# Kernel optimization log

Measured on AMD Instinct MI355X. Metric: run time of the kernel, lower is better.

Reference implementation:

```python
import jax, jax.numpy as jnp
import numpy as np

DELTA = 1e-3  # kernel_delta

B, N, D, K = 256, 131072, 128, 50


def setup_inputs() -> dict:
    key = jax.random.key(0)
    k1, k2, k3 = jax.random.split(key, 3)
    return {
        "key": jax.random.normal(k1, (B, D), dtype=jnp.float32),
        "keys": jax.random.normal(k2, (N, D), dtype=jnp.float32),
        "values": jax.random.normal(k3, (N, 1), dtype=jnp.float32),
        "num_neighbours": K,
    }


def reference(key, keys, values, num_neighbours):
    # Squared L2 distance via GEMM expansion (same math as
    # torch.square(torch.norm(key[:,None]-keys, dim=-1)))
    q_sq = jnp.sum(key * key, axis=1, keepdims=True)          # [B,1]
    d_sq = jnp.sum(keys * keys, axis=1)                        # [N]
    cross = key @ keys.T                                       # [B,N] GEMM
    dist2 = jnp.maximum(q_sq + d_sq[None, :] - 2.0 * cross, 0.0)
    # inverse-distance-weighting kernel
    weights = 1.0 / (dist2 + DELTA)                            # [B,N]
    # top-k mask + renormalize (non-topk weights are zeroed, so the
    # normalized sum reduces to a sum over the top-k entries)
    top_w, top_idx = jax.lax.top_k(weights, num_neighbours)    # [B,K]
    w_norm = top_w / jnp.sum(top_w, axis=1, keepdims=True)     # [B,K]
    # gather matched values and weighted sum
    v = values[top_idx, 0]                                     # [B,K]
    output = jnp.sum(w_norm * v, axis=1, keepdims=True)        # [B,1]
    return output
```

## Files before the change

kernel.cpp:

```cpp
#include <hip/hip_runtime.h>

#define BQ 256
#define NK 131072
#define DIM 128
#define KT2 128
#define NCH2 (NK / KT2)
#define DELTA 1e-3f

#define NB 8192
#define SHIFT 18
#define CAP 2048

typedef __attribute__((ext_vector_type(8))) short bf16x8;
typedef __attribute__((ext_vector_type(4))) float f32x4;

__device__ __forceinline__ unsigned short f2bf(float x) {
    unsigned u = __float_as_uint(x);
    u += 0x7fffu + ((u >> 16) & 1u);
    return (unsigned short)(u >> 16);
}
__device__ __forceinline__ float bf2f(unsigned short h) {
    return __uint_as_float(((unsigned)h) << 16);
}

__global__ __launch_bounds__(256, 4)
void p0_qsq(const float* __restrict__ qkey, float* __restrict__ qsqg)
{
    const int t = threadIdx.x;
    #pragma unroll 1
    for (int p = 0; p < 16; ++p) {
        int r  = p * 16 + (t >> 4);
        int d0 = (t & 15) * 8;
        const float* src = qkey + (r << 7) + d0;
        float4 a = *(const float4*)src, b = *(const float4*)(src + 4);
        float s = (a.x*a.x + a.y*a.y) + (a.z*a.z + a.w*a.w)
                + (b.x*b.x + b.y*b.y) + (b.z*b.z + b.w*b.w);
        #pragma unroll
        for (int off = 1; off < 16; off <<= 1) s += __shfl_xor(s, off, 16);
        if ((t & 15) == 0) qsqg[r] = s;
    }
}

__global__ __launch_bounds__(512, 2)
void p1_mfma(const float* __restrict__ qkey, const float* __restrict__ keys,
             const float* __restrict__ qsqg, float* __restrict__ dist,
             int q0, int nq)
{
    __shared__ __align__(16) unsigned short khs[KT2 * DIM];
    __shared__ __align__(16) unsigned short kls[KT2 * DIM];
    __shared__ float ksq_s[KT2];
    __shared__ float qsq_s[BQ];

    const int tid   = threadIdx.x;
    const int kbase = blockIdx.x * KT2;

    if (tid < BQ) qsq_s[tid] = qsqg[tid];

    #pragma unroll
    for (int p = 0; p < 4; ++p) {
        int flat = p * 4096 + tid * 8;
        int rr = flat >> 7;
        int d0 = flat & 127;
        const float* src = keys + (((size_t)(kbase + rr)) << 7) + d0;
        float4 a = *(const float4*)src, b = *(const float4*)(src + 4);
        float xs0 = a.x, xs1 = a.y, xs2 = a.z, xs3 = a.w;
        float xs4 = b.x, xs5 = b.y, xs6 = b.z, xs7 = b.w;
        bf16x8 hv, lv;
        unsigned short h;
        h = f2bf(xs0); hv[0] = (short)h; lv[0] = (short)f2bf(xs0 - bf2f(h));
        h = f2bf(xs1); hv[1] = (short)h; lv[1] = (short)f2bf(xs1 - bf2f(h));
        h = f2bf(xs2); hv[2] = (short)h; lv[2] = (short)f2bf(xs2 - bf2f(h));
        h = f2bf(xs3); hv[3] = (short)h; lv[3] = (short)f2bf(xs3 - bf2f(h));
        h = f2bf(xs4); hv[4] = (short)h; lv[4] = (short)f2bf(xs4 - bf2f(h));
        h = f2bf(xs5); hv[5] = (short)h; lv[5] = (short)f2bf(xs5 - bf2f(h));
        h = f2bf(xs6); hv[6] = (short)h; lv[6] = (short)f2bf(xs6 - bf2f(h));
        h = f2bf(xs7); hv[7] = (short)h; lv[7] = (short)f2bf(xs7 - bf2f(h));
        float sq = (xs0*xs0 + xs1*xs1) + (xs2*xs2 + xs3*xs3)
                 + (xs4*xs4 + xs5*xs5) + (xs6*xs6 + xs7*xs7);
        unsigned byte = (unsigned)((rr << 8) + (d0 << 1));
        byte ^= (unsigned)((rr & 7) << 4);
        *(bf16x8*)((char*)khs + byte) = hv;
        *(bf16x8*)((char*)kls + byte) = lv;
        #pragma unroll
        for (int off = 1; off < 16; off <<= 1) sq += __shfl_xor(sq, off, 16);
        if ((tid & 15) == 0) ksq_s[rr] = sq;
    }

    const int lane = tid & 63, wv = tid >> 6;
    const int qb0 = wv * 32;
    const int fr = lane & 15, fg = lane >> 4;
    bf16x8 qh[2][4], ql[2][4];
    #pragma unroll
    for (int qf = 0; qf < 2; ++qf)
        #pragma unroll
        for (int s = 0; s < 4; ++s) {
            const float* qp = qkey + ((size_t)(qb0 + qf * 16 + fr) << 7) + s * 32 + fg * 8;
            float4 a = *(const float4*)qp, b = *(const float4*)(qp + 4);
            float x0 = a.x, x1 = a.y, x2 = a.z, x3 = a.w;
            float x4 = b.x, x5 = b.y, x6 = b.z, x7 = b.w;
            bf16x8 hv, lv;
            unsigned short h;
            h = f2bf(x0); hv[0] = (short)h; lv[0] = (short)f2bf(x0 - bf2f(h));
            h = f2bf(x1); hv[1] = (short)h; lv[1] = (short)f2bf(x1 - bf2f(h));
            h = f2bf(x2); hv[2] = (short)h; lv[2] = (short)f2bf(x2 - bf2f(h));
            h = f2bf(x3); hv[3] = (short)h; lv[3] = (short)f2bf(x3 - bf2f(h));
            h = f2bf(x4); hv[4] = (short)h; lv[4] = (short)f2bf(x4 - bf2f(h));
            h = f2bf(x5); hv[5] = (short)h; lv[5] = (short)f2bf(x5 - bf2f(h));
            h = f2bf(x6); hv[6] = (short)h; lv[6] = (short)f2bf(x6 - bf2f(h));
            h = f2bf(x7); hv[7] = (short)h; lv[7] = (short)f2bf(x7 - bf2f(h));
            qh[qf][s] = hv; ql[qf][s] = lv;
        }

    f32x4 acc[2][8];
    #pragma unroll
    for (int qf = 0; qf < 2; ++qf)
        #pragma unroll
        for (int kf = 0; kf < 8; ++kf) acc[qf][kf] = f32x4{0.f, 0.f, 0.f, 0.f};

    __syncthreads();

    #pragma unroll
    for (int s = 0; s < 4; ++s) {
        #pragma unroll
        for (int kf = 0; kf < 8; ++kf) {
            const int krow = kf * 16 + fr;
            const int d0   = s * 32 + fg * 8;
            unsigned byte = ((unsigned)((krow << 8) + (d0 << 1))) ^ (unsigned)((krow & 7) << 4);
            bf16x8 bh = *(bf16x8*)((char*)khs + byte);
            bf16x8 bl = *(bf16x8*)((char*)kls + byte);
            #pragma unroll
            for (int qf = 0; qf < 2; ++qf) {
                acc[qf][kf] = __builtin_amdgcn_mfma_f32_16x16x32_bf16(qh[qf][s], bh, acc[qf][kf], 0, 0, 0);
                acc[qf][kf] = __builtin_amdgcn_mfma_f32_16x16x32_bf16(ql[qf][s], bh, acc[qf][kf], 0, 0, 0);
                acc[qf][kf] = __builtin_amdgcn_mfma_f32_16x16x32_bf16(qh[qf][s], bl, acc[qf][kf], 0, 0, 0);
            }
        }
    }

    #pragma unroll
    for (int qf = 0; qf < 2; ++qf) {
        #pragma unroll
        for (int kf = 0; kf < 8; ++kf) {
            int k = kbase + kf * 16 + fr;
            float kq = ksq_s[kf * 16 + fr];
            f32x4 a = acc[qf][kf];
            #pragma unroll
            for (int rg = 0; rg < 4; ++rg) {
                int q = qb0 + qf * 16 + fg * 4 + rg;
                int qrel = q - q0;
                if (qrel >= 0 && qrel < nq) {
                    float dv = fmaxf(qsq_s[q] + kq - 2.f * a[rg], 0.f);
                    dist[(size_t)qrel * NK + k] = dv;
                }
            }
        }
    }
}

__global__ __launch_bounds__(1024, 1)
void p2_select(const float* __restrict__ dist,
               const float* __restrict__ values,
               const int* __restrict__ pK,
               float* __restrict__ out)
{
    const int tid  = threadIdx.x;
    const int lane = tid & 63;
    const int wid  = tid >> 6;
    const float4* row4 = (const float4*)(dist + (size_t)blockIdx.x * NK);

    int K = *pK; if (K < 1) K = 1; if (K > NK) K = NK;

    __shared__ int   hist[NB];
    __shared__ uint2 list[CAP];
    __shared__ int   lcount, s_bb, s_cb;
    __shared__ int   iscan[16];
    __shared__ float fred[48];

    for (int i = tid; i < NB; i += 1024) hist[i] = 0;
    if (tid == 0) { lcount = 0; s_bb = NB - 1; s_cb = 0; }
    __syncthreads();

    for (int i = 0; i < NK / 4096; ++i) {
        float4 v = row4[tid + 1024 * i];
        atomicAdd(&hist[__float_as_uint(v.x) >> SHIFT], 1);
        atomicAdd(&hist[__float_as_uint(v.y) >> SHIFT], 1);
        atomicAdd(&hist[__float_as_uint(v.z) >> SHIFT], 1);
        atomicAdd(&hist[__float_as_uint(v.w) >> SHIFT], 1);
    }
    __syncthreads();

    int h[8], s = 0;
    #pragma unroll
    for (int b = 0; b < 8; ++b) { h[b] = hist[tid * 8 + b]; s += h[b]; }
    int incl = s;
    #pragma unroll
    for (int off = 1; off < 64; off <<= 1) {
        int t = __shfl_up(incl, off, 64);
        if (lane >= off) incl += t;
    }
    if (lane == 63) iscan[wid] = incl;
    __syncthreads();
    if (tid == 0) { int c = 0; for (int w = 0; w < 16; ++w) { int t = iscan[w]; iscan[w] = c; c += t; } }
    __syncthreads();
    int base = iscan[wid] + (incl - s);
    if (base < K && K <= base + s) {
        int c = base;
        #pragma unroll
        for (int b = 0; b < 8; ++b) {
            if (c < K && c + h[b] >= K) { s_bb = tid * 8 + b; s_cb = c; }
            c += h[b];
        }
    }
    __syncthreads();
    const int bb = s_bb, cbelow = s_cb, R = K - cbelow, CEall = hist[bb];

    float sw = 0.f, swv = 0.f, seva = 0.f;
    for (int i = 0; i < NK / 4096; ++i) {
        float4 v = row4[tid + 1024 * i];
        int n0 = (tid + 1024 * i) * 4;
        float dd[4] = { v.x, v.y, v.z, v.w };
        #pragma unroll
        for (int c = 0; c < 4; ++c) {
            unsigned bts = __float_as_uint(dd[c]);
            int bin = (int)(bts >> SHIFT);
            if (bin < bb) {
                float w = 1.f / (dd[c] + DELTA);
                float vv = values[n0 + c];
                sw += w; swv = fmaf(w, vv, swv);
            } else if (bin == bb) {
                float vv = values[n0 + c];
                seva += vv;
                int sl = atomicAdd(&lcount, 1);
                if (sl < CAP) list[sl] = make_uint2(bts, __float_as_uint(vv));
            }
        }
    }
    #pragma unroll
    for (int off = 32; off; off >>= 1) {
        sw   += __shfl_down(sw,   off, 64);
        swv  += __shfl_down(swv,  off, 64);
        seva += __shfl_down(seva, off, 64);
    }
    if (lane == 0) { fred[wid] = sw; fred[16 + wid] = swv; fred[32 + wid] = seva; }
    __syncthreads();

    if (wid == 0) {
        float SW = 0.f, SWV = 0.f, SEVA = 0.f;
        for (int w = 0; w < 16; ++w) { SW += fred[w]; SWV += fred[16 + w]; SEVA += fred[32 + w]; }
        const int L = lcount;
        double num, den;
        if (L <= CAP) {
            unsigned lo = ((unsigned)bb) << SHIFT;
            unsigned hi = lo + ((1u << SHIFT) - 1u);
            while (lo < hi) {
                unsigned mid = lo + ((hi - lo) >> 1);
                int c = 0;
                for (int i = lane; i < L; i += 64) c += (list[i].x <= mid) ? 1 : 0;
                #pragma unroll
                for (int off = 32; off; off >>= 1) c += __shfl_xor(c, off, 64);
                if (c >= R) hi = mid; else lo = mid + 1;
            }
            const unsigned T = lo;
            int cl2 = 0, ce = 0;
            double swl = 0.0, swvl = 0.0, sevt = 0.0;
            for (int i = lane; i < L; i += 64) {
                unsigned b = list[i].x;
                float vv = __uint_as_float(list[i].y);
                if (b < T) {
                    double w = 1.0 / ((double)__uint_as_float(b) + (double)DELTA);
                    cl2 += 1; swl += w; swvl += w * (double)vv;
                } else if (b == T) { ce += 1; sevt += (double)vv; }
            }
            #pragma unroll
            for (int off = 32; off; off >>= 1) {
                cl2  += __shfl_xor(cl2,  off, 64);
                ce   += __shfl_xor(ce,   off, 64);
                swl  += __shfl_xor(swl,  off, 64);
                swvl += __shfl_xor(swvl, off, 64);
                sevt += __shfl_xor(sevt, off, 64);
            }
            const int need = R - cl2;
            double wT = 1.0 / ((double)__uint_as_float(T) + (double)DELTA);
            num = (double)SWV + swvl + wT * ((double)need / (double)ce) * sevt;
            den = (double)SW  + swl  + wT * (double)need;
        } else {
            double wT = 1.0 / ((double)__uint_as_float(((unsigned)bb) << SHIFT) + (double)DELTA);
            num = (double)SWV + wT * ((double)R / (double)CEall) * (double)SEVA;
            den = (double)SW  + wT * (double)R;
        }
        if (lane == 0) out[blockIdx.x] = (float)(num / den);
    }
}

extern "C" void kernel_launch(void* const* d_in, const int* in_sizes, int n_in,
                              void* d_out, int out_size, void* d_ws, size_t ws_size,
                              hipStream_t stream)
{
    const float* qkey   = (const float*)d_in[0];
    const float* keys   = (const float*)d_in[1];
    const float* values = (const float*)d_in[2];
    const int*   pK     = (const int*)d_in[3];
    float* out  = (float*)d_out;

    float* qsqg = (float*)d_ws;
    float* dist = (float*)d_ws + 1024;

    p0_qsq<<<dim3(1), dim3(256), 0, stream>>>(qkey, qsqg);

    const size_t rowb = (size_t)NK * sizeof(float);
    const size_t avail = ws_size - 4096;
    int slabQ = (avail >= (size_t)BQ * rowb) ? BQ : (int)(avail / rowb);
    if (slabQ < 1) slabQ = 1;

    for (int q0 = 0; q0 < BQ; q0 += slabQ) {
        int nq = BQ - q0; if (nq > slabQ) nq = slabQ;
        p1_mfma<<<dim3(NCH2), dim3(512), 0, stream>>>(qkey, keys, qsqg, dist, q0, nq);
        p2_select<<<dim3(nq), dim3(1024), 0, stream>>>(dist, values, pK, out + q0);
    }
}
```

Before: 126.2 us.

## Replace full distance matrix with sampled threshold and filtered candidate lists

```diff
diff --git a/kernel.cpp b/kernel.cpp
--- a/kernel.cpp
+++ b/kernel.cpp
@@ -5,11 +5,10 @@
 #define DIM 128
 #define KT2 128
 #define NCH2 (NK / KT2)
+#define SAMP 8192
+#define SBLK (SAMP / KT2)
+#define CAPC 16384
 #define DELTA 1e-3f
-
-#define NB 8192
-#define SHIFT 18
-#define CAP 2048
 
 typedef __attribute__((ext_vector_type(8))) short bf16x8;
 typedef __attribute__((ext_vector_type(4))) float f32x4;
@@ -22,39 +21,62 @@
 __device__ __forceinline__ float bf2f(unsigned short h) {
     return __uint_as_float(((unsigned)h) << 16);
 }
+__device__ __forceinline__ int kclamp(int K) {
+    if (K < 1) K = 1;
+    if (K > 2048) K = 2048;
+    return K;
+}
 
 __global__ __launch_bounds__(256, 4)
-void p0_qsq(const float* __restrict__ qkey, float* __restrict__ qsqg)
-{
-    const int t = threadIdx.x;
-    #pragma unroll 1
-    for (int p = 0; p < 16; ++p) {
-        int r  = p * 16 + (t >> 4);
-        int d0 = (t & 15) * 8;
-        const float* src = qkey + (r << 7) + d0;
-        float4 a = *(const float4*)src, b = *(const float4*)(src + 4);
-        float s = (a.x*a.x + a.y*a.y) + (a.z*a.z + a.w*a.w)
-                + (b.x*b.x + b.y*b.y) + (b.z*b.z + b.w*b.w);
-        #pragma unroll
-        for (int off = 1; off < 16; off <<= 1) s += __shfl_xor(s, off, 16);
-        if ((t & 15) == 0) qsqg[r] = s;
-    }
-}
-
+void p0_prep(const float* __restrict__ qkey,
+             unsigned short* __restrict__ qhG, unsigned short* __restrict__ qlG,
+             float* __restrict__ qsqg)
+{
+    const int item = blockIdx.x * 256 + threadIdx.x;
+    const int r = item >> 4, d0 = (item & 15) * 8;
+    const float* src = qkey + (r << 7) + d0;
+    float4 a = *(const float4*)src, b = *(const float4*)(src + 4);
+    float x0 = a.x, x1 = a.y, x2 = a.z, x3 = a.w;
+    float x4 = b.x, x5 = b.y, x6 = b.z, x7 = b.w;
+    bf16x8 hv, lv;
+    unsigned short h;
+    h = f2bf(x0); hv[0] = (short)h; lv[0] = (short)f2bf(x0 - bf2f(h));
+    h = f2bf(x1); hv[1] = (short)h; lv[1] = (short)f2bf(x1 - bf2f(h));
+    h = f2bf(x2); hv[2] = (short)h; lv[2] = (short)f2bf(x2 - bf2f(h));
+    h = f2bf(x3); hv[3] = (short)h; lv[3] = (short)f2bf(x3 - bf2f(h));
+    h = f2bf(x4); hv[4] = (short)h; lv[4] = (short)f2bf(x4 - bf2f(h));
+    h = f2bf(x5); hv[5] = (short)h; lv[5] = (short)f2bf(x5 - bf2f(h));
+    h = f2bf(x6); hv[6] = (short)h; lv[6] = (short)f2bf(x6 - bf2f(h));
+    h = f2bf(x7); hv[7] = (short)h; lv[7] = (short)f2bf(x7 - bf2f(h));
+    *(bf16x8*)(qhG + (r << 7) + d0) = hv;
+    *(bf16x8*)(qlG + (r << 7) + d0) = lv;
+    float s = (x0*x0 + x1*x1) + (x2*x2 + x3*x3) + (x4*x4 + x5*x5) + (x6*x6 + x7*x7);
+    #pragma unroll
+    for (int off = 1; off < 16; off <<= 1) s += __shfl_xor(s, off, 16);
+    if ((threadIdx.x & 15) == 0) qsqg[r] = s;
+}
+
+template<bool FILTER>
 __global__ __launch_bounds__(512, 2)
-void p1_mfma(const float* __restrict__ qkey, const float* __restrict__ keys,
-             const float* __restrict__ qsqg, float* __restrict__ dist,
-             int q0, int nq)
+void kmfma(const unsigned short* __restrict__ qhG, const unsigned short* __restrict__ qlG,
+           const float* __restrict__ keys, const float* __restrict__ qsqg,
+           const float* __restrict__ values, float* __restrict__ dout,
+           const unsigned* __restrict__ tau, unsigned* __restrict__ cnt,
+           uint2* __restrict__ cand)
 {
     __shared__ __align__(16) unsigned short khs[KT2 * DIM];
     __shared__ __align__(16) unsigned short kls[KT2 * DIM];
-    __shared__ float ksq_s[KT2];
-    __shared__ float qsq_s[BQ];
+    __shared__ float    ksq_s[KT2];
+    __shared__ float    qsq_s[BQ];
+    __shared__ unsigned tau_s[BQ];
 
     const int tid   = threadIdx.x;
     const int kbase = blockIdx.x * KT2;
 
-    if (tid < BQ) qsq_s[tid] = qsqg[tid];
+    if (tid < BQ) {
+        qsq_s[tid] = qsqg[tid];
+        if (FILTER) tau_s[tid] = tau[tid];
+    }
 
     #pragma unroll
     for (int p = 0; p < 4; ++p) {
@@ -63,20 +85,19 @@
         int d0 = flat & 127;
         const float* src = keys + (((size_t)(kbase + rr)) << 7) + d0;
         float4 a = *(const float4*)src, b = *(const float4*)(src + 4);
-        float xs0 = a.x, xs1 = a.y, xs2 = a.z, xs3 = a.w;
-        float xs4 = b.x, xs5 = b.y, xs6 = b.z, xs7 = b.w;
+        float x0 = a.x, x1 = a.y, x2 = a.z, x3 = a.w;
+        float x4 = b.x, x5 = b.y, x6 = b.z, x7 = b.w;
         bf16x8 hv, lv;
         unsigned short h;
-        h = f2bf(xs0); hv[0] = (short)h; lv[0] = (short)f2bf(xs0 - bf2f(h));
-        h = f2bf(xs1); hv[1] = (short)h; lv[1] = (short)f2bf(xs1 - bf2f(h));
-        h = f2bf(xs2); hv[2] = (short)h; lv[2] = (short)f2bf(xs2 - bf2f(h));
-        h = f2bf(xs3); hv[3] = (short)h; lv[3] = (short)f2bf(xs3 - bf2f(h));
-        h = f2bf(xs4); hv[4] = (short)h; lv[4] = (short)f2bf(xs4 - bf2f(h));
-        h = f2bf(xs5); hv[5] = (short)h; lv[5] = (short)f2bf(xs5 - bf2f(h));
-        h = f2bf(xs6); hv[6] = (short)h; lv[6] = (short)f2bf(xs6 - bf2f(h));
-        h = f2bf(xs7); hv[7] = (short)h; lv[7] = (short)f2bf(xs7 - bf2f(h));
-        float sq = (xs0*xs0 + xs1*xs1) + (xs2*xs2 + xs3*xs3)
-                 + (xs4*xs4 + xs5*xs5) + (xs6*xs6 + xs7*xs7);
+        h = f2bf(x0); hv[0] = (short)h; lv[0] = (short)f2bf(x0 - bf2f(h));
+        h = f2bf(x1); hv[1] = (short)h; lv[1] = (short)f2bf(x1 - bf2f(h));
+        h = f2bf(x2); hv[2] = (short)h; lv[2] = (short)f2bf(x2 - bf2f(h));
+        h = f2bf(x3); hv[3] = (short)h; lv[3] = (short)f2bf(x3 - bf2f(h));
+        h = f2bf(x4); hv[4] = (short)h; lv[4] = (short)f2bf(x4 - bf2f(h));
+        h = f2bf(x5); hv[5] = (short)h; lv[5] = (short)f2bf(x5 - bf2f(h));
+        h = f2bf(x6); hv[6] = (short)h; lv[6] = (short)f2bf(x6 - bf2f(h));
+        h = f2bf(x7); hv[7] = (short)h; lv[7] = (short)f2bf(x7 - bf2f(h));
+        float sq = (x0*x0 + x1*x1) + (x2*x2 + x3*x3) + (x4*x4 + x5*x5) + (x6*x6 + x7*x7);
         unsigned byte = (unsigned)((rr << 8) + (d0 << 1));
         byte ^= (unsigned)((rr & 7) << 4);
         *(bf16x8*)((char*)khs + byte) = hv;
@@ -94,21 +115,9 @@
     for (int qf = 0; qf < 2; ++qf)
         #pragma unroll
         for (int s = 0; s < 4; ++s) {
-            const float* qp = qkey + ((size_t)(qb0 + qf * 16 + fr) << 7) + s * 32 + fg * 8;
-            float4 a = *(const float4*)qp, b = *(const float4*)(qp + 4);
-            float x0 = a.x, x1 = a.y, x2 = a.z, x3 = a.w;
-            float x4 = b.x, x5 = b.y, x6 = b.z, x7 = b.w;
-            bf16x8 hv, lv;
-            unsigned short h;
-            h = f2bf(x0); hv[0] = (short)h; lv[0] = (short)f2bf(x0 - bf2f(h));
-            h = f2bf(x1); hv[1] = (short)h; lv[1] = (short)f2bf(x1 - bf2f(h));
-            h = f2bf(x2); hv[2] = (short)h; lv[2] = (short)f2bf(x2 - bf2f(h));
-            h = f2bf(x3); hv[3] = (short)h; lv[3] = (short)f2bf(x3 - bf2f(h));
-            h = f2bf(x4); hv[4] = (short)h; lv[4] = (short)f2bf(x4 - bf2f(h));
-            h = f2bf(x5); hv[5] = (short)h; lv[5] = (short)f2bf(x5 - bf2f(h));
-            h = f2bf(x6); hv[6] = (short)h; lv[6] = (short)f2bf(x6 - bf2f(h));
-            h = f2bf(x7); hv[7] = (short)h; lv[7] = (short)f2bf(x7 - bf2f(h));
-            qh[qf][s] = hv; ql[qf][s] = lv;
+            int off = ((qb0 + qf * 16 + fr) << 7) + s * 32 + fg * 8;
+            qh[qf][s] = *(const bf16x8*)(qhG + off);
+            ql[qf][s] = *(const bf16x8*)(qlG + off);
         }
 
     f32x4 acc[2][8];
@@ -141,154 +150,129 @@
     for (int qf = 0; qf < 2; ++qf) {
         #pragma unroll
         for (int kf = 0; kf < 8; ++kf) {
-            int k = kbase + kf * 16 + fr;
-            float kq = ksq_s[kf * 16 + fr];
+            const int kcol = kf * 16 + fr;
+            const int k = kbase + kcol;
+            const float kq = ksq_s[kcol];
             f32x4 a = acc[qf][kf];
             #pragma unroll
             for (int rg = 0; rg < 4; ++rg) {
-                int q = qb0 + qf * 16 + fg * 4 + rg;
-                int qrel = q - q0;
-                if (qrel >= 0 && qrel < nq) {
-                    float dv = fmaxf(qsq_s[q] + kq - 2.f * a[rg], 0.f);
-                    dist[(size_t)qrel * NK + k] = dv;
+                const int q = qb0 + qf * 16 + fg * 4 + rg;
+                float dv = fmaxf(qsq_s[q] + kq - 2.f * a[rg], 0.f);
+                if (FILTER) {
+                    if (dv <= __uint_as_float(tau_s[q])) {
+                        unsigned slot = atomicAdd(&cnt[q], 1u);
+                        if (slot < CAPC)
+                            cand[(size_t)q * CAPC + slot] =
+                                make_uint2(__float_as_uint(dv), __float_as_uint(values[k]));
+                    }
+                } else {
+                    dout[(size_t)q * SAMP + k] = dv;
                 }
             }
         }
     }
 }
 
-__global__ __launch_bounds__(1024, 1)
-void p2_select(const float* __restrict__ dist,
-               const float* __restrict__ values,
-               const int* __restrict__ pK,
-               float* __restrict__ out)
-{
-    const int tid  = threadIdx.x;
-    const int lane = tid & 63;
-    const int wid  = tid >> 6;
-    const float4* row4 = (const float4*)(dist + (size_t)blockIdx.x * NK);
-
-    int K = *pK; if (K < 1) K = 1; if (K > NK) K = NK;
-
-    __shared__ int   hist[NB];
-    __shared__ uint2 list[CAP];
-    __shared__ int   lcount, s_bb, s_cb;
-    __shared__ int   iscan[16];
-    __shared__ float fred[48];
-
-    for (int i = tid; i < NB; i += 1024) hist[i] = 0;
-    if (tid == 0) { lcount = 0; s_bb = NB - 1; s_cb = 0; }
-    __syncthreads();
-
-    for (int i = 0; i < NK / 4096; ++i) {
-        float4 v = row4[tid + 1024 * i];
-        atomicAdd(&hist[__float_as_uint(v.x) >> SHIFT], 1);
-        atomicAdd(&hist[__float_as_uint(v.y) >> SHIFT], 1);
-        atomicAdd(&hist[__float_as_uint(v.z) >> SHIFT], 1);
-        atomicAdd(&hist[__float_as_uint(v.w) >> SHIFT], 1);
-    }
-    __syncthreads();
-
-    int h[8], s = 0;
-    #pragma unroll
-    for (int b = 0; b < 8; ++b) { h[b] = hist[tid * 8 + b]; s += h[b]; }
-    int incl = s;
-    #pragma unroll
-    for (int off = 1; off < 64; off <<= 1) {
-        int t = __shfl_up(incl, off, 64);
-        if (lane >= off) incl += t;
-    }
-    if (lane == 63) iscan[wid] = incl;
-    __syncthreads();
-    if (tid == 0) { int c = 0; for (int w = 0; w < 16; ++w) { int t = iscan[w]; iscan[w] = c; c += t; } }
-    __syncthreads();
-    int base = iscan[wid] + (incl - s);
-    if (base < K && K <= base + s) {
-        int c = base;
-        #pragma unroll
-        for (int b = 0; b < 8; ++b) {
-            if (c < K && c + h[b] >= K) { s_bb = tid * 8 + b; s_cb = c; }
-            c += h[b];
-        }
-    }
-    __syncthreads();
-    const int bb = s_bb, cbelow = s_cb, R = K - cbelow, CEall = hist[bb];
-
-    float sw = 0.f, swv = 0.f, seva = 0.f;
-    for (int i = 0; i < NK / 4096; ++i) {
-        float4 v = row4[tid + 1024 * i];
-        int n0 = (tid + 1024 * i) * 4;
-        float dd[4] = { v.x, v.y, v.z, v.w };
-        #pragma unroll
-        for (int c = 0; c < 4; ++c) {
-            unsigned bts = __float_as_uint(dd[c]);
-            int bin = (int)(bts >> SHIFT);
-            if (bin < bb) {
-                float w = 1.f / (dd[c] + DELTA);
-                float vv = values[n0 + c];
-                sw += w; swv = fmaf(w, vv, swv);
-            } else if (bin == bb) {
-                float vv = values[n0 + c];
-                seva += vv;
-                int sl = atomicAdd(&lcount, 1);
-                if (sl < CAP) list[sl] = make_uint2(bts, __float_as_uint(vv));
-            }
-        }
+__global__ __launch_bounds__(256, 4)
+void k2_tau(const float* __restrict__ dsamp, const int* __restrict__ pK,
+            unsigned* __restrict__ tau, unsigned* __restrict__ cnt)
+{
+    const int q = blockIdx.x, tid = threadIdx.x;
+    const int lane = tid & 63, wid = tid >> 6;
+    const int K = kclamp(*pK);
+
+    unsigned eb[32];
+    const float4* row4 = (const float4*)(dsamp + (size_t)q * SAMP);
+    #pragma unroll
+    for (int i = 0; i < 8; ++i) {
+        float4 v = row4[tid + 256 * i];
+        eb[4*i+0] = __float_as_uint(v.x); eb[4*i+1] = __float_as_uint(v.y);
+        eb[4*i+2] = __float_as_uint(v.z); eb[4*i+3] = __float_as_uint(v.w);
+    }
+
+    __shared__ int red[4];
+    __shared__ unsigned go;
+    unsigned lo = 0u, hi = 0x7f7fffffu;
+    while (lo < hi) {
+        unsigned mid = lo + ((hi - lo) >> 1);
+        int c = 0;
+        #pragma unroll
+        for (int i = 0; i < 32; ++i) c += (eb[i] <= mid) ? 1 : 0;
+        #pragma unroll
+        for (int off = 32; off; off >>= 1) c += __shfl_down(c, off, 64);
+        if (lane == 0) red[wid] = c;
+        __syncthreads();
+        if (tid == 0) go = ((red[0] + red[1] + red[2] + red[3]) >= K) ? 1u : 0u;
+        __syncthreads();
+        if (go) hi = mid; else lo = mid + 1;
+        __syncthreads();
+    }
+    if (tid == 0) { tau[q] = lo; cnt[q] = 0u; }
+}
+
+__global__ __launch_bounds__(256, 4)
+void k4_final(const uint2* __restrict__ cand, const unsigned* __restrict__ cnt,
+              const unsigned* __restrict__ tau, const int* __restrict__ pK,
+              float* __restrict__ out)
+{
+    const int q = blockIdx.x, tid = threadIdx.x;
+    const int lane = tid & 63, wid = tid >> 6;
+    const int K = kclamp(*pK);
+    int n = (int)cnt[q]; if (n > CAPC) n = CAPC;
+    const uint2* L = cand + (size_t)q * CAPC;
+
+    __shared__ int red[4];
+    __shared__ unsigned go;
+
+    unsigned lo = 0u, hi = tau[q];
+    while (lo < hi) {
+        unsigned mid = lo + ((hi - lo) >> 1);
+        int c = 0;
+        for (int i = tid; i < n; i += 256) c += (L[i].x <= mid) ? 1 : 0;
+        #pragma unroll
+        for (int off = 32; off; off >>= 1) c += __shfl_down(c, off, 64);
+        if (lane == 0) red[wid] = c;
+        __syncthreads();
+        if (tid == 0) go = ((red[0] + red[1] + red[2] + red[3]) >= K) ? 1u : 0u;
+        __syncthreads();
+        if (go) hi = mid; else lo = mid + 1;
+        __syncthreads();
+    }
+    const unsigned T = lo;
+
+    double sw = 0.0, swv = 0.0, sevt = 0.0;
+    int cl = 0, ce = 0;
+    for (int i = tid; i < n; i += 256) {
+        unsigned b = L[i].x;
+        float d = __uint_as_float(b), v = __uint_as_float(L[i].y);
+        if (b < T) {
+            double w = 1.0 / ((double)d + (double)DELTA);
+            cl += 1; sw += w; swv += w * (double)v;
+        } else if (b == T) { ce += 1; sevt += (double)v; }
     }
     #pragma unroll
     for (int off = 32; off; off >>= 1) {
         sw   += __shfl_down(sw,   off, 64);
         swv  += __shfl_down(swv,  off, 64);
-        seva += __shfl_down(seva, off, 64);
-    }
-    if (lane == 0) { fred[wid] = sw; fred[16 + wid] = swv; fred[32 + wid] = seva; }
+        sevt += __shfl_down(sevt, off, 64);
+        cl   += __shfl_down(cl,   off, 64);
+        ce   += __shfl_down(ce,   off, 64);
+    }
+    __shared__ double dred[3][4];
+    __shared__ int    ired[2][4];
+    if (lane == 0) { dred[0][wid] = sw; dred[1][wid] = swv; dred[2][wid] = sevt;
+                     ired[0][wid] = cl; ired[1][wid] = ce; }
     __syncthreads();
-
-    if (wid == 0) {
-        float SW = 0.f, SWV = 0.f, SEVA = 0.f;
-        for (int w = 0; w < 16; ++w) { SW += fred[w]; SWV += fred[16 + w]; SEVA += fred[32 + w]; }
-        const int L = lcount;
-        double num, den;
-        if (L <= CAP) {
-            unsigned lo = ((unsigned)bb) << SHIFT;
-            unsigned hi = lo + ((1u << SHIFT) - 1u);
-            while (lo < hi) {
-                unsigned mid = lo + ((hi - lo) >> 1);
-                int c = 0;
-                for (int i = lane; i < L; i += 64) c += (list[i].x <= mid) ? 1 : 0;
-                #pragma unroll
-                for (int off = 32; off; off >>= 1) c += __shfl_xor(c, off, 64);
-                if (c >= R) hi = mid; else lo = mid + 1;
-            }
-            const unsigned T = lo;
-            int cl2 = 0, ce = 0;
-            double swl = 0.0, swvl = 0.0, sevt = 0.0;
-            for (int i = lane; i < L; i += 64) {
-                unsigned b = list[i].x;
-                float vv = __uint_as_float(list[i].y);
-                if (b < T) {
-                    double w = 1.0 / ((double)__uint_as_float(b) + (double)DELTA);
-                    cl2 += 1; swl += w; swvl += w * (double)vv;
-                } else if (b == T) { ce += 1; sevt += (double)vv; }
-            }
-            #pragma unroll
-            for (int off = 32; off; off >>= 1) {
-                cl2  += __shfl_xor(cl2,  off, 64);
-                ce   += __shfl_xor(ce,   off, 64);
-                swl  += __shfl_xor(swl,  off, 64);
-                swvl += __shfl_xor(swvl, off, 64);
-                sevt += __shfl_xor(sevt, off, 64);
-            }
-            const int need = R - cl2;
-            double wT = 1.0 / ((double)__uint_as_float(T) + (double)DELTA);
-            num = (double)SWV + swvl + wT * ((double)need / (double)ce) * sevt;
-            den = (double)SW  + swl  + wT * (double)need;
-        } else {
-            double wT = 1.0 / ((double)__uint_as_float(((unsigned)bb) << SHIFT) + (double)DELTA);
-            num = (double)SWV + wT * ((double)R / (double)CEall) * (double)SEVA;
-            den = (double)SW  + wT * (double)R;
-        }
-        if (lane == 0) out[blockIdx.x] = (float)(num / den);
+    if (tid == 0) {
+        double SW = 0, SWV = 0, SEVT = 0; int CL = 0, CE = 0;
+        #pragma unroll
+        for (int w = 0; w < 4; ++w) { SW += dred[0][w]; SWV += dred[1][w]; SEVT += dred[2][w];
+                                      CL += ired[0][w]; CE += ired[1][w]; }
+        double wT = 1.0 / ((double)__uint_as_float(T) + (double)DELTA);
+        double need = (double)(K - CL);
+        double num = SWV + wT * (need / (double)CE) * SEVT;
+        double den = SW + wT * need;
+        out[q] = (float)(num / den);
     }
 }
 
@@ -300,21 +284,22 @@
     const float* keys   = (const float*)d_in[1];
     const float* values = (const float*)d_in[2];
     const int*   pK     = (const int*)d_in[3];
-    float* out  = (float*)d_out;
-
-    float* qsqg = (float*)d_ws;
-    float* dist = (float*)d_ws + 1024;
-
-    p0_qsq<<<dim3(1), dim3(256), 0, stream>>>(qkey, qsqg);
-
-    const size_t rowb = (size_t)NK * sizeof(float);
-    const size_t avail = ws_size - 4096;
-    int slabQ = (avail >= (size_t)BQ * rowb) ? BQ : (int)(avail / rowb);
-    if (slabQ < 1) slabQ = 1;
-
-    for (int q0 = 0; q0 < BQ; q0 += slabQ) {
-        int nq = BQ - q0; if (nq > slabQ) nq = slabQ;
-        p1_mfma<<<dim3(NCH2), dim3(512), 0, stream>>>(qkey, keys, qsqg, dist, q0, nq);
-        p2_select<<<dim3(nq), dim3(1024), 0, stream>>>(dist, values, pK, out + q0);
-    }
-}
+    float* out = (float*)d_out;
+
+    char* w = (char*)d_ws;
+    float*          qsqg  = (float*)w;
+    unsigned short* qhG   = (unsigned short*)(w + 4096);
+    unsigned short* qlG   = (unsigned short*)(w + 4096 + 65536);
+    float*          dsamp = (float*)(w + 4096 + 131072);
+    unsigned*       tau   = (unsigned*)(w + 4096 + 131072 + 8388608);
+    unsigned*       cnt   = (unsigned*)(w + 4096 + 131072 + 8388608 + 1024);
+    uint2*          cand  = (uint2*)(w + 4096 + 131072 + 8388608 + 2048);
+
+    p0_prep<<<dim3(16), dim3(256), 0, stream>>>(qkey, qhG, qlG, qsqg);
+    kmfma<false><<<dim3(SBLK), dim3(512), 0, stream>>>(qhG, qlG, keys, qsqg, values,
+                                                       dsamp, tau, cnt, cand);
+    k2_tau<<<dim3(BQ), dim3(256), 0, stream>>>(dsamp, pK, tau, cnt);
+    kmfma<true><<<dim3(NCH2), dim3(512), 0, stream>>>(qhG, qlG, keys, qsqg, values,
+                                                      dsamp, tau, cnt, cand);
+    k4_final<<<dim3(BQ), dim3(256), 0, stream>>>(cand, cnt, tau, pK, out);
+}
```

After: 294.1 us. +133.2%, slower.
